# Kernel tuning notes

Measured on AMD Instinct MI355X. Metric: run time of the kernel, lower is better.

Reference implementation:

```python
import jax, jax.numpy as jnp
import numpy as np

HIDDEN = 128
INPUT_DIM = 50000


def setup_inputs() -> dict:
    key = jax.random.key(0)
    ks = jax.random.split(key, 9)
    h = HIDDEN
    d = INPUT_DIM

    def lin_init(k, shape, fan_in):
        # equinox Linear/GRUCell default: U(-1/sqrt(fan_in), 1/sqrt(fan_in))
        lim = 1.0 / np.sqrt(fan_in)
        return jax.random.uniform(k, shape, minval=-lim, maxval=lim, dtype=jnp.float32)

    return {
        "x0": jax.random.normal(ks[0], (d,), dtype=jnp.float32),
        "W_enc": lin_init(ks[1], (h, d), d),
        "b_enc": lin_init(ks[2], (h,), d),
        "W_ih": lin_init(ks[3], (3 * h, h), h),
        "W_hh": lin_init(ks[4], (3 * h, h), h),
        "b_ih": lin_init(ks[5], (3 * h,), h),
        "b_n": lin_init(ks[6], (h,), h),
        "W_dec": lin_init(ks[7], (d, h), h),
        "b_dec": lin_init(ks[8], (d,), h),
        "steps": 100,
    }


def _gru_cell(x, h_prev, W_ih, W_hh, b_ih, b_n):
    # equinox eqx.nn.GRUCell math
    ig = jnp.split(W_ih @ x + b_ih, 3)
    hg = jnp.split(W_hh @ h_prev, 3)
    reset = jax.nn.sigmoid(ig[0] + hg[0])
    inp = jax.nn.sigmoid(ig[1] + hg[1])
    new = jnp.tanh(ig[2] + reset * (hg[2] + b_n))
    return new + inp * (h_prev - new)


def reference(x0, W_enc, b_enc, W_ih, W_hh, b_ih, b_n, W_dec, b_dec, steps):
    h0 = jnp.zeros((HIDDEN,), dtype=x0.dtype)

    def scan_step(carry, _):
        h, x_prev = carry
        embedded = W_enc @ x_prev + b_enc            # [hidden]
        h_new = _gru_cell(embedded, h, W_ih, W_hh, b_ih, b_n)
        x_next = W_dec @ h_new + b_dec               # [input_dim]
        return (h_new, x_next), (x_next, x_next, jnp.zeros_like(x_next))

    _, (samples, means, sigmas) = jax.lax.scan(scan_step, (h0, x0), None, length=steps)
    return samples, means, sigmas
```

## Files before the change

### kernel.cpp

```cpp
#include <hip/hip_runtime.h>
#include <math.h>

#define HIDDEN 128
#define IDIM   50000
#define STEPS  100

typedef _Float16 half_t;
typedef _Float16 h2_t __attribute__((ext_vector_type(2)));

#define WS_E1H  0
#define WS_CH   256
#define WS_M    512
#define WS_P    16896
#define WS_Q    66048
#define WS_IG1  66432
#define WS_HT   66816

#define SC_PART 0
#define SC_MP   9000000

__global__ __launch_bounds__(256, 2) void k_encgemm(const float* __restrict__ W_enc,
    const float* __restrict__ W_dec, const float* __restrict__ x0,
    const float* __restrict__ b_dec, float* __restrict__ ws,
    float* __restrict__ scratch)
{
  __shared__ __align__(16) float smem[1024];
  const int t = threadIdx.x;

  if (blockIdx.x < 500){
    float (*As)[128] = (float(*)[128])smem;
    float (*Bs)[128] = (float(*)[128])(smem + 512);
    const int tx = t & 15, ty = t >> 4;
    const int d0 = blockIdx.x * 100;
    const int u  = t - 128, ukk = u >> 5, ug = u & 31;
    float acc[8][8];
    #pragma unroll
    for (int p = 0; p < 8; p++)
      #pragma unroll
      for (int q = 0; q < 8; q++) acc[p][q] = 0.f;

    float4 stage;
    if (t < 128) stage = *(const float4*)(W_enc + (size_t)t*IDIM + d0);
    else         stage = *(const float4*)(W_dec + (size_t)(d0+ukk)*HIDDEN + ug*4);

    for (int k0 = 0; k0 < 100; k0 += 4){
      if (t < 128){
        As[0][t] = stage.x; As[1][t] = stage.y; As[2][t] = stage.z; As[3][t] = stage.w;
      } else {
        *(float4*)&Bs[ukk][ug*4] = stage;
      }
      __syncthreads();
      if (k0 + 4 < 100){
        if (t < 128) stage = *(const float4*)(W_enc + (size_t)t*IDIM + d0 + k0 + 4);
        else         stage = *(const float4*)(W_dec + (size_t)(d0+k0+4+ukk)*HIDDEN + ug*4);
      }
      #pragma unroll
      for (int kk = 0; kk < 4; kk++){
        float4 alo = *(const float4*)&As[kk][ty*8];
        float4 ahi = *(const float4*)&As[kk][ty*8+4];
        float4 blo = *(const float4*)&Bs[kk][tx*8];
        float4 bhi = *(const float4*)&Bs[kk][tx*8+4];
        float a[8] = {alo.x,alo.y,alo.z,alo.w,ahi.x,ahi.y,ahi.z,ahi.w};
        float b[8] = {blo.x,blo.y,blo.z,blo.w,bhi.x,bhi.y,bhi.z,bhi.w};
        #pragma unroll
        for (int p = 0; p < 8; p++)
          #pragma unroll
          for (int q = 0; q < 8; q++) acc[p][q] += a[p]*b[q];
      }
      __syncthreads();
    }
    float* outp = scratch + (size_t)blockIdx.x * 16384;
    #pragma unroll
    for (int p = 0; p < 8; p++){
      #pragma unroll
      for (int q = 0; q < 8; q += 4){
        *(float4*)&outp[(ty*8+p)*128 + tx*8 + q] =
          make_float4(acc[p][q], acc[p][q+1], acc[p][q+2], acc[p][q+3]);
      }
    }
  } else {
    const int bid  = blockIdx.x - 500;
    const int r    = bid >> 1;
    const int half = bid & 1;
    float* r0 = smem;
    float* r1 = smem + 256;
    const float4* wr = (const float4*)(W_enc + (size_t)r*IDIM + half*25000);
    const float4* xv = (const float4*)(x0   + half*25000);
    const float4* bv = (const float4*)(b_dec + half*25000);
    float s0 = 0.f, s1 = 0.f;
    for (int i = t; i < 6250; i += 256){
      float4 w = wr[i]; float4 a = xv[i]; float4 b = bv[i];
      s0 += w.x*a.x + w.y*a.y + w.z*a.z + w.w*a.w;
      s1 += w.x*b.x + w.y*b.y + w.z*b.z + w.w*b.w;
    }
    r0[t] = s0; r1[t] = s1;
    __syncthreads();
    for (int off = 128; off > 0; off >>= 1){
      if (t < off){ r0[t] += r0[t+off]; r1[t] += r1[t+off]; }
      __syncthreads();
    }
    if (t == 0){
      ws[WS_E1H + half*128 + r] = r0[0];
      ws[WS_CH  + half*128 + r] = r1[0];
    }
  }
}

__global__ __launch_bounds__(256) void k_reduce1(const float* __restrict__ scratch,
    float* __restrict__ Mp)
{
  const int g     = blockIdx.x % 10;
  const int chunk = blockIdx.x / 10;
  const int idx   = chunk * 256 + threadIdx.x;
  const float* base = scratch + (size_t)(g*50) * 16384 + idx;
  float s[10];
  #pragma unroll
  for (int uu = 0; uu < 10; uu++) s[uu] = 0.f;
  for (int p = 0; p < 50; p += 10){
    #pragma unroll
    for (int uu = 0; uu < 10; uu++)
      s[uu] += base[(size_t)(p+uu)*16384];
  }
  float t0 = (s[0]+s[1]) + (s[2]+s[3]);
  float t1 = (s[4]+s[5]) + (s[6]+s[7]);
  Mp[(size_t)g*16384 + idx] = t0 + t1 + (s[8]+s[9]);
}

__global__ __launch_bounds__(256) void k_reduce2(const float* __restrict__ Mp,
    float* __restrict__ Mout)
{
  const int idx = blockIdx.x * 256 + threadIdx.x;
  float s = 0.f;
  #pragma unroll
  for (int g = 0; g < 10; g++) s += Mp[(size_t)g*16384 + idx];
  Mout[idx] = s;
}

__global__ __launch_bounds__(128) void k_smallP(const float* __restrict__ W_ih,
    const float* __restrict__ b_ih, const float* __restrict__ b_enc,
    const float* __restrict__ ws, const float* __restrict__ M,
    float* __restrict__ P, float* __restrict__ q, float* __restrict__ ig1)
{
  const int r = blockIdx.x, j = threadIdx.x;
  const float* wr = W_ih + (size_t)r * HIDDEN;
  float acc = 0.f;
  #pragma unroll 8
  for (int k = 0; k < HIDDEN; k++) acc += wr[k] * M[k*HIDDEN + j];
  P[(size_t)r*HIDDEN + j] = acc;
  const float wj = wr[j];
  float cj  = ws[WS_CH  + j] + ws[WS_CH  + 128 + j];
  float e1j = ws[WS_E1H + j] + ws[WS_E1H + 128 + j];
  float t0 = wj * (cj  + b_enc[j]);
  float t1 = wj * (e1j + b_enc[j]);
  __shared__ float r0[128], r1[128];
  r0[j] = t0; r1[j] = t1;
  __syncthreads();
  for (int off = 64; off > 0; off >>= 1){
    if (j < off){ r0[j] += r0[j+off]; r1[j] += r1[j+off]; }
    __syncthreads();
  }
  if (j == 0){
    q[r]   = r0[0] + b_ih[r];
    ig1[r] = r1[0] + b_ih[r];
  }
}

__device__ __forceinline__ float fexp2_(float x){ return __builtin_amdgcn_exp2f(x); }
__device__ __forceinline__ float frcp_(float x){ return __builtin_amdgcn_rcpf(x); }
__device__ __forceinline__ float fsig_(float x){
  return frcp_(1.f + fexp2_(x * -1.44269504f));
}
__device__ __forceinline__ float ftanh_(float x){
  return 1.f - 2.f * frcp_(fexp2_(x * 2.88539008f) + 1.f);
}
__device__ __forceinline__ float dppx1_(float x){
  return __builtin_bit_cast(float,
      __builtin_amdgcn_mov_dpp(__builtin_bit_cast(int, x), 0xB1, 0xF, 0xF, true));
}

__global__
__attribute__((amdgpu_flat_work_group_size(256, 256), amdgpu_waves_per_eu(1, 1)))
void k_recur(const float* __restrict__ P,
    const float* __restrict__ W_hh, const float* __restrict__ q,
    const float* __restrict__ b_n, const float* __restrict__ ig1,
    float* __restrict__ H_T)
{
  const int t = threadIdx.x;
  const int e = t >> 1;
  const int p = t & 1;

  const float* s0 = p ? (P    + (size_t)(128 + e) * HIDDEN)
                      : (P    + (size_t)e         * HIDDEN);
  const float* s1 = p ? (W_hh + (size_t)e         * HIDDEN)
                      : (P    + (size_t)(256 + e) * HIDDEN);
  const float* s2 = p ? (W_hh + (size_t)(256 + e) * HIDDEN)
                      : (W_hh + (size_t)(128 + e) * HIDDEN);
  const float a_init = p ? q[128 + e] : q[e];
  const float b_init = p ? 0.f        : q[256 + e];

  h2_t wa[64], wb[64], wc[64];
  {
    const float4* f0 = (const float4*)s0;
    const float4* f1 = (const float4*)s1;
    const float4* f2 = (const float4*)s2;
    #pragma unroll
    for (int j = 0; j < 32; j++){
      float4 v0 = f0[j], v1 = f1[j], v2 = f2[j];
      h2_t w;
      w.x=(half_t)v0.x; w.y=(half_t)v0.y; wa[2*j]   = w;
      w.x=(half_t)v0.z; w.y=(half_t)v0.w; wa[2*j+1] = w;
      w.x=(half_t)v1.x; w.y=(half_t)v1.y; wb[2*j]   = w;
      w.x=(half_t)v1.z; w.y=(half_t)v1.w; wb[2*j+1] = w;
      w.x=(half_t)v2.x; w.y=(half_t)v2.y; wc[2*j]   = w;
      w.x=(half_t)v2.z; w.y=(half_t)v2.w; wc[2*j+1] = w;
    }
  }

  __shared__ __align__(16) half_t h16[2][HIDDEN];
  __shared__ float Hs[128 * 101];

  const float bn = b_n[e];
  float h;
  {
    float reset = fsig_(ig1[e]);
    float inp   = fsig_(ig1[128 + e]);
    float nw    = ftanh_(ig1[256 + e] + reset * bn);
    h = nw - inp * nw;
  }
  if (!p) h16[0][e] = (half_t)h;
  else    Hs[e * 101] = h;
  __syncthreads();

#define RSTEP(KK, RD, WR)                                                     \
  {                                                                           \
    const uint4* hq = (const uint4*)(h16[RD]);                                \
    float a0 = a_init, a1 = 0.f;                                              \
    float b0 = b_init, b1 = 0.f;                                              \
    float c0 = 0.f,    c1 = 0.f;                                              \
    _Pragma("unroll")                                                         \
    for (int jj = 0; jj < 16; jj++){                                          \
      uint4 hb = hq[jj];                                                      \
      h2_t hx = __builtin_bit_cast(h2_t, hb.x);                               \
      h2_t hy = __builtin_bit_cast(h2_t, hb.y);                               \
      h2_t hz = __builtin_bit_cast(h2_t, hb.z);                               \
      h2_t hw = __builtin_bit_cast(h2_t, hb.w);                               \
      a0 = __builtin_amdgcn_fdot2(wa[4*jj+0], hx, a0, false);                 \
      a1 = __builtin_amdgcn_fdot2(wa[4*jj+1], hy, a1, false);                 \
      a0 = __builtin_amdgcn_fdot2(wa[4*jj+2], hz, a0, false);                 \
      a1 = __builtin_amdgcn_fdot2(wa[4*jj+3], hw, a1, false);                 \
      b0 = __builtin_amdgcn_fdot2(wb[4*jj+0], hx, b0, false);                 \
      b1 = __builtin_amdgcn_fdot2(wb[4*jj+1], hy, b1, false);                 \
      b0 = __builtin_amdgcn_fdot2(wb[4*jj+2], hz, b0, false);                 \
      b1 = __builtin_amdgcn_fdot2(wb[4*jj+3], hw, b1, false);                 \
      c0 = __builtin_amdgcn_fdot2(wc[4*jj+0], hx, c0, false);                 \
      c1 = __builtin_amdgcn_fdot2(wc[4*jj+1], hy, c1, false);                 \
      c0 = __builtin_amdgcn_fdot2(wc[4*jj+2], hz, c0, false);                 \
      c1 = __builtin_amdgcn_fdot2(wc[4*jj+3], hw, c1, false);                 \
    }                                                                         \
    float A = a0 + a1, B = b0 + b1, C = c0 + c1;                              \
    float An = dppx1_(A), Bn = dppx1_(B), Cn = dppx1_(C);                     \
    \
    float igr = p ? An : A;                                                   \
    float igi = p ? A  : An;                                                  \
    float hgr = p ? B  : Bn;                                                  \
    float ign = p ? Bn : B;                                                   \
    float hgi = p ? Cn : C;                                                   \
    float hgn = p ? C  : Cn;                                                  \
    float rs = fsig_(igr + hgr);                                              \
    float ip = fsig_(igi + hgi);                                              \
    float nw = ftanh_(ign + rs * (hgn + bn));                                 \
    h = nw + ip * (h - nw);                                                   \
    if (!p) h16[WR][e] = (half_t)h;                                           \
    else    Hs[e * 101 + (KK)] = h;                                           \
    __syncthreads();                                                          \
  }

  for (int k = 1; k < STEPS - 1; k += 2){
    RSTEP(k,     0, 1);
    RSTEP(k + 1, 1, 0);
  }
  RSTEP(STEPS - 1, 0, 1);
#undef RSTEP

  for (int i = 0; i < 64; i++){
    int f = i * 256 + t;
    int ee = f >> 7, kk = f & 127;
    H_T[f] = (kk < STEPS) ? Hs[ee * 101 + kk] : 0.f;
  }
}

__global__ __launch_bounds__(256, 4) void k_decode(const float* __restrict__ W_dec,
    const float* __restrict__ b_dec, const float* __restrict__ H_T,
    float* __restrict__ out)
{
  __shared__ __align__(16) float Bs[128][132];
  const int t  = threadIdx.x;
  const int tx = t & 15, ty = t >> 4;
  const int d0 = blockIdx.x * 64;

  for (int l = t; l < 4096; l += 256){
    int j = l >> 5, g = l & 31;
    *(float4*)&Bs[j][g*4] = *(const float4*)&H_T[(size_t)j*HIDDEN + g*4];
  }
  __syncthreads();

  const int d  = d0 + tx*4;
  const int dc = (d < IDIM) ? d : 0;
  const float* A0 = W_dec + (size_t)dc * HIDDEN;
  const float* A1 = A0 + HIDDEN;
  const float* A2 = A1 + HIDDEN;
  const float* A3 = A2 + HIDDEN;

  float acc[4][8];
  #pragma unroll
  for (int p = 0; p < 4; p++)
    #pragma unroll
    for (int q = 0; q < 8; q++) acc[p][q] = 0.f;

  for (int j0 = 0; j0 < HIDDEN; j0 += 4){
    float4 a0 = *(const float4*)(A0 + j0);
    float4 a1 = *(const float4*)(A1 + j0);
    float4 a2 = *(const float4*)(A2 + j0);
    float4 a3 = *(const float4*)(A3 + j0);
    #pragma unroll
    for (int jj = 0; jj < 4; jj++){
      float4 b0 = *(const float4*)&Bs[j0+jj][ty*8];
      float4 b1 = *(const float4*)&Bs[j0+jj][ty*8+4];
      float e0 = (jj==0)?a0.x:(jj==1)?a0.y:(jj==2)?a0.z:a0.w;
      float e1 = (jj==0)?a1.x:(jj==1)?a1.y:(jj==2)?a1.z:a1.w;
      float e2 = (jj==0)?a2.x:(jj==1)?a2.y:(jj==2)?a2.z:a2.w;
      float e3 = (jj==0)?a3.x:(jj==1)?a3.y:(jj==2)?a3.z:a3.w;
      acc[0][0]+=e0*b0.x; acc[0][1]+=e0*b0.y; acc[0][2]+=e0*b0.z; acc[0][3]+=e0*b0.w;
      acc[0][4]+=e0*b1.x; acc[0][5]+=e0*b1.y; acc[0][6]+=e0*b1.z; acc[0][7]+=e0*b1.w;
      acc[1][0]+=e1*b0.x; acc[1][1]+=e1*b0.y; acc[1][2]+=e1*b0.z; acc[1][3]+=e1*b0.w;
      acc[1][4]+=e1*b1.x; acc[1][5]+=e1*b1.y; acc[1][6]+=e1*b1.z; acc[1][7]+=e1*b1.w;
      acc[2][0]+=e2*b0.x; acc[2][1]+=e2*b0.y; acc[2][2]+=e2*b0.z; acc[2][3]+=e2*b0.w;
      acc[2][4]+=e2*b1.x; acc[2][5]+=e2*b1.y; acc[2][6]+=e2*b1.z; acc[2][7]+=e2*b1.w;
      acc[3][0]+=e3*b0.x; acc[3][1]+=e3*b0.y; acc[3][2]+=e3*b0.z; acc[3][3]+=e3*b0.w;
      acc[3][4]+=e3*b1.x; acc[3][5]+=e3*b1.y; acc[3][6]+=e3*b1.z; acc[3][7]+=e3*b1.w;
    }
  }

  if (d < IDIM){
    float4 bd = *(const float4*)&b_dec[d];
    const size_t SO = (size_t)STEPS * IDIM;
    #pragma unroll
    for (int qq = 0; qq < 8; qq++){
      int k = ty*8 + qq;
      if (k < STEPS){
        float4 v = make_float4(acc[0][qq]+bd.x, acc[1][qq]+bd.y,
                               acc[2][qq]+bd.z, acc[3][qq]+bd.w);
        size_t o = (size_t)k * IDIM + d;
        *(float4*)&out[o]        = v;
        *(float4*)&out[o + SO]   = v;
        *(float4*)&out[o + 2*SO] = make_float4(0.f,0.f,0.f,0.f);
      }
    }
  }
}

extern "C" void kernel_launch(void* const* d_in, const int* in_sizes, int n_in,
                              void* d_out, int out_size, void* d_ws, size_t ws_size,
                              hipStream_t stream) {
  const float* x0    = (const float*)d_in[0];
  const float* W_enc = (const float*)d_in[1];
  const float* b_enc = (const float*)d_in[2];
  const float* W_ih  = (const float*)d_in[3];
  const float* W_hh  = (const float*)d_in[4];
  const float* b_ih  = (const float*)d_in[5];
  const float* b_n   = (const float*)d_in[6];
  const float* W_dec = (const float*)d_in[7];
  const float* b_dec = (const float*)d_in[8];
  (void)in_sizes; (void)n_in; (void)out_size; (void)ws_size;

  float* out = (float*)d_out;
  float* ws  = (float*)d_ws;
  float* M   = ws + WS_M;
  float* P   = ws + WS_P;
  float* q   = ws + WS_Q;
  float* ig1 = ws + WS_IG1;
  float* H_T = ws + WS_HT;
  float* scratch = out + SC_PART;
  float* Mp      = out + SC_MP;

  hipLaunchKernelGGL(k_encgemm, dim3(756), dim3(256), 0, stream, W_enc, W_dec, x0, b_dec, ws, scratch);
  hipLaunchKernelGGL(k_reduce1, dim3(640), dim3(256), 0, stream, scratch, Mp);
  hipLaunchKernelGGL(k_reduce2, dim3(64),  dim3(256), 0, stream, Mp, M);
  hipLaunchKernelGGL(k_smallP,  dim3(384), dim3(128), 0, stream, W_ih, b_ih, b_enc, ws, M, P, q, ig1);
  hipLaunchKernelGGL(k_recur,   dim3(1),   dim3(256), 0, stream, P, W_hh, q, b_n, ig1, H_T);
  hipLaunchKernelGGL(k_decode,  dim3(782), dim3(256), 0, stream, W_dec, b_dec, H_T, out);
}
```

Baseline: 298.2 us.

## Stage W_dec tile in LDS and read H_T from global in decode GEMM

The decode kernel now loads its 64-row W_dec tile into shared memory with coalesced float4 loads, instead of each thread streaming four strided W_dec rows from global memory. H_T is now read directly from global memory, relying on cache since all blocks share it. Threads are remapped to rows tx+16p, so the output stores become scalar writes coalesced across tx rather than float4 writes. This aims to improve W_dec load coalescing, but it trades away vector stores and adds global or L2 traffic for H_T inside the inner loop.

After: 267.5 us. 1.11x faster.

```diff
diff --git a/kernel.cpp b/kernel.cpp
--- a/kernel.cpp
+++ b/kernel.cpp
@@ -259,7 +259,6 @@
     }                                                                         \
     float A = a0 + a1, B = b0 + b1, C = c0 + c1;                              \
     float An = dppx1_(A), Bn = dppx1_(B), Cn = dppx1_(C);                     \
-    \
     float igr = p ? An : A;                                                   \
     float igi = p ? A  : An;                                                  \
     float hgr = p ? B  : Bn;                                                  \
@@ -293,24 +292,22 @@
     const float* __restrict__ b_dec, const float* __restrict__ H_T,
     float* __restrict__ out)
 {
-  __shared__ __align__(16) float Bs[128][132];
+  __shared__ __align__(16) float Ws[64][132];
   const int t  = threadIdx.x;
   const int tx = t & 15, ty = t >> 4;
   const int d0 = blockIdx.x * 64;
 
-  for (int l = t; l < 4096; l += 256){
-    int j = l >> 5, g = l & 31;
-    *(float4*)&Bs[j][g*4] = *(const float4*)&H_T[(size_t)j*HIDDEN + g*4];
+  #pragma unroll
+  for (int i = 0; i < 8; i++){
+    int f4 = i * 256 + t;
+    int rl = f4 >> 5;
+    int cl = (f4 & 31) * 4;
+    int rg = d0 + rl;
+    float4 v = *(const float4*)&W_dec[(size_t)((rg < IDIM) ? rg : 0)*HIDDEN + cl];
+    *(float4*)&Ws[rl][cl] = v;
   }
   __syncthreads();
 
-  const int d  = d0 + tx*4;
-  const int dc = (d < IDIM) ? d : 0;
-  const float* A0 = W_dec + (size_t)dc * HIDDEN;
-  const float* A1 = A0 + HIDDEN;
-  const float* A2 = A1 + HIDDEN;
-  const float* A3 = A2 + HIDDEN;
-
   float acc[4][8];
   #pragma unroll
   for (int p = 0; p < 4; p++)
@@ -318,14 +315,15 @@
     for (int q = 0; q < 8; q++) acc[p][q] = 0.f;
 
   for (int j0 = 0; j0 < HIDDEN; j0 += 4){
-    float4 a0 = *(const float4*)(A0 + j0);
-    float4 a1 = *(const float4*)(A1 + j0);
-    float4 a2 = *(const float4*)(A2 + j0);
-    float4 a3 = *(const float4*)(A3 + j0);
+    float4 a0 = *(const float4*)&Ws[tx     ][j0];
+    float4 a1 = *(const float4*)&Ws[tx + 16][j0];
+    float4 a2 = *(const float4*)&Ws[tx + 32][j0];
+    float4 a3 = *(const float4*)&Ws[tx + 48][j0];
     #pragma unroll
     for (int jj = 0; jj < 4; jj++){
-      float4 b0 = *(const float4*)&Bs[j0+jj][ty*8];
-      float4 b1 = *(const float4*)&Bs[j0+jj][ty*8+4];
+      const float* hrow = H_T + (size_t)(j0 + jj) * HIDDEN + ty * 8;
+      float4 b0 = *(const float4*)hrow;
+      float4 b1 = *(const float4*)(hrow + 4);
       float e0 = (jj==0)?a0.x:(jj==1)?a0.y:(jj==2)?a0.z:a0.w;
       float e1 = (jj==0)?a1.x:(jj==1)?a1.y:(jj==2)?a1.z:a1.w;
       float e2 = (jj==0)?a2.x:(jj==1)?a2.y:(jj==2)?a2.z:a2.w;
@@ -341,19 +339,27 @@
     }
   }
 
-  if (d < IDIM){
-    float4 bd = *(const float4*)&b_dec[d];
-    const size_t SO = (size_t)STEPS * IDIM;
-    #pragma unroll
-    for (int qq = 0; qq < 8; qq++){
-      int k = ty*8 + qq;
-      if (k < STEPS){
-        float4 v = make_float4(acc[0][qq]+bd.x, acc[1][qq]+bd.y,
-                               acc[2][qq]+bd.z, acc[3][qq]+bd.w);
-        size_t o = (size_t)k * IDIM + d;
-        *(float4*)&out[o]        = v;
-        *(float4*)&out[o + SO]   = v;
-        *(float4*)&out[o + 2*SO] = make_float4(0.f,0.f,0.f,0.f);
+  bool dv[4]; float bd[4];
+  #pragma unroll
+  for (int p = 0; p < 4; p++){
+    int d = d0 + tx + 16*p;
+    dv[p] = (d < IDIM);
+    bd[p] = dv[p] ? b_dec[d] : 0.f;
+  }
+  const size_t SO = (size_t)STEPS * IDIM;
+  #pragma unroll
+  for (int qq = 0; qq < 8; qq++){
+    int k = ty*8 + qq;
+    if (k < STEPS){
+      size_t o = (size_t)k * IDIM + d0 + tx;
+      #pragma unroll
+      for (int p = 0; p < 4; p++){
+        if (dv[p]){
+          float v = acc[p][qq] + bd[p];
+          out[o + 16*p]          = v;
+          out[o + 16*p + SO]     = v;
+          out[o + 16*p + 2*SO]   = 0.f;
+        }
       }
     }
   }
```
